# Optimization experiments

Measured on AMD Instinct MI355X. Metric: run time of the kernel, lower is better.

## Reference

```python
import jax, jax.numpy as jnp
import numpy as np

NEG_SLOPE = 0.2  # PyG GATConv default leaky_relu slope
EPS = 1e-16


def setup_inputs() -> dict:
    key = jax.random.key(0)
    ks = jax.random.split(key, 6)
    N, F, H, C, E = 50000, 128, 8, 16, 600000
    node_features = jax.random.normal(ks[0], (N, F), dtype=jnp.float32)
    edge_index = jax.random.randint(ks[1], (2, E), 0, N, dtype=jnp.int64)
    W = jax.random.normal(ks[2], (F, H * C), dtype=jnp.float32) * (1.0 / np.sqrt(F))
    att_src = jax.random.normal(ks[3], (H, C), dtype=jnp.float32)
    att_dst = jax.random.normal(ks[4], (H, C), dtype=jnp.float32)
    bias = jnp.zeros((H * C,), dtype=jnp.float32)
    return {"node_features": node_features, "edge_index": edge_index,
            "W": W, "att_src": att_src, "att_dst": att_dst, "bias": bias}


def reference(node_features, edge_index, W, att_src, att_dst, bias):
    N = node_features.shape[0]
    H, C = att_src.shape
    # Linear transform, split into heads: [N, H, C]
    x = (node_features @ W).reshape(N, H, C)
    # add self loops (PyG default add_self_loops=True)
    loop = jnp.arange(N, dtype=edge_index.dtype)
    src = jnp.concatenate([edge_index[0], loop])  # message source j
    dst = jnp.concatenate([edge_index[1], loop])  # message target i
    # per-node attention logits [N, H]
    a_src = jnp.einsum('nhc,hc->nh', x, att_src)
    a_dst = jnp.einsum('nhc,hc->nh', x, att_dst)
    # edge-wise logits with leaky relu [E, H]
    alpha = jax.nn.leaky_relu(a_src[src] + a_dst[dst], NEG_SLOPE)
    # softmax over incoming edges of each target node (segment softmax)
    amax = jax.ops.segment_max(alpha, dst, num_segments=N)
    alpha = jnp.exp(alpha - amax[dst])
    asum = jax.ops.segment_sum(alpha, dst, num_segments=N)
    alpha = alpha / (asum[dst] + EPS)
    # weighted scatter-aggregate of source features [N, H, C]
    msgs = x[src] * alpha[:, :, None]
    out = jax.ops.segment_sum(msgs, dst, num_segments=N)
    out = out.reshape(N, H * C) + bias
    # SELU activation; dropout is identity in eval mode
    return jax.nn.selu(out)
```

## Files before the change

kernel.cpp:

```cpp
#include <hip/hip_runtime.h>
#include <hip/hip_fp16.h>

#define LEAKY_SLOPE 0.2f

typedef _Float16 h8 __attribute__((ext_vector_type(8)));
typedef float f32x4 __attribute__((ext_vector_type(4)));

__device__ __forceinline__ float leaky_relu_f(float v) { return v > 0.f ? v : LEAKY_SLOPE * v; }
__device__ __forceinline__ float selu_f(float v) {
    const float sc = 1.0507009873554805f, al = 1.6732632423543772f;
    return v > 0.f ? sc * v : sc * al * expm1f(v);
}

__device__ __forceinline__ int detect_is64_wave(const int* __restrict__ e32) {
    int v = e32[2 * (threadIdx.x & 63) + 1];
    unsigned long long b = __ballot(v != 0);
    return b == 0ull ? 1 : 0;
}

__device__ __forceinline__ int edge_at(const void* edges, long long idx, int is64) {
    return is64 ? (int)((const long long*)edges)[idx] : ((const int*)edges)[idx];
}

__global__ void prep_kernel(int* __restrict__ deg, int n,
                            const float* __restrict__ W, _Float16* __restrict__ Wt,
                            int* __restrict__ state, int nstate) {
    int i = blockIdx.x * blockDim.x + threadIdx.x;
    if (i < n) deg[i] = 0;
    if (i < nstate) state[i] = 0;
    if (i < 128 * 128) {
        int k = i >> 7, c = i & 127;
        Wt[c * 128 + k] = (_Float16)W[i];
    }
}

__global__ __launch_bounds__(256) void gemmhist_kernel(
    const float* __restrict__ feats, const _Float16* __restrict__ Wt,
    const float* __restrict__ att_src, const float* __restrict__ att_dst,
    __half* __restrict__ xh, float* __restrict__ a_src, float* __restrict__ a_dst,
    int N, int gemmBlocks,
    const void* __restrict__ edges, long long E,
    int* __restrict__ deg, int* __restrict__ rank) {
    __shared__ __align__(16) _Float16 Af[64][136];
    __shared__ __align__(16) _Float16 Bt[128][136];
    const int t = threadIdx.x;

    if ((int)blockIdx.x >= gemmBlocks) {
        int is64 = detect_is64_wave((const int*)edges);
        long long hstride = (long long)(gridDim.x - gemmBlocks) * blockDim.x;
        for (long long e = (long long)((int)blockIdx.x - gemmBlocks) * blockDim.x + t;
             e < E; e += hstride) {
            int dst = edge_at(edges, E + e, is64);
            rank[e] = atomicAdd(&deg[dst], 1);
        }
        return;
    }

    const int bid = blockIdx.x;
    if (bid == 0) {
        if (t < 64) *(__half2*)&xh[(long long)N * 128 + 2 * t] = __floats2half2_rn(0.f, 0.f);
        if (t < 8) a_src[N * 8 + t] = -1e30f;
    }

    {
        const float4* F4 = (const float4*)feats;
#pragma unroll
        for (int i = 0; i < 8; i++) {
            int q = t + i * 256;
            int row = q >> 5;
            int c = (q & 31) * 4;
            int r_abs = bid * 64 + row;
            if (r_abs >= N) r_abs = N - 1;
            float4 v = F4[(long long)r_abs * 32 + (q & 31)];
            union { _Float16 h[4]; uint2 u; } tmp;
            tmp.h[0] = (_Float16)v.x; tmp.h[1] = (_Float16)v.y;
            tmp.h[2] = (_Float16)v.z; tmp.h[3] = (_Float16)v.w;
            *(uint2*)&Af[row][c] = tmp.u;
        }
    }
    {
        const uint4* Wt4 = (const uint4*)Wt;
#pragma unroll
        for (int i = 0; i < 8; i++) {
            int q = t + i * 256;
            int c = q >> 4;
            int k0 = (q & 15) * 8;
            *(uint4*)&Bt[c][k0] = Wt4[q];
        }
    }
    __syncthreads();

    const int l = t & 63;
    const int w = t >> 6;
    const int lr = l & 15;
    const int lg = l >> 4;

    f32x4 acc[8];
#pragma unroll
    for (int n = 0; n < 8; n++) acc[n] = (f32x4){0.f, 0.f, 0.f, 0.f};

#pragma unroll
    for (int kk = 0; kk < 4; kk++) {
        const int k0 = kk * 32 + lg * 8;
        h8 a = *(const h8*)&Af[16 * w + lr][k0];
#pragma unroll
        for (int n = 0; n < 8; n++) {
            h8 b = *(const h8*)&Bt[16 * n + lr][k0];
            acc[n] = __builtin_amdgcn_mfma_f32_16x16x32_f16(a, b, acc[n], 0, 0, 0);
        }
    }

    const int rbase = bid * 64 + 16 * w + lg * 4;
#pragma unroll
    for (int n = 0; n < 8; n++) {
        float asv = att_src[n * 16 + lr];
        float adv = att_dst[n * 16 + lr];
#pragma unroll
        for (int r = 0; r < 4; r++) {
            int row_abs = rbase + r;
            float v = acc[n][r];
            if (row_abs < N) xh[(long long)row_abs * 128 + 16 * n + lr] = (__half)v;
            float ps = v * asv;
            float pd = v * adv;
            ps += __shfl_xor(ps, 1); ps += __shfl_xor(ps, 2);
            ps += __shfl_xor(ps, 4); ps += __shfl_xor(ps, 8);
            pd += __shfl_xor(pd, 1); pd += __shfl_xor(pd, 2);
            pd += __shfl_xor(pd, 4); pd += __shfl_xor(pd, 8);
            if (lr == n && row_abs < N) {
                a_src[row_abs * 8 + n] = ps;
                a_dst[row_abs * 8 + n] = pd;
            }
        }
    }
}

__global__ __launch_bounds__(256) void scanlb_kernel(const int* __restrict__ deg,
                                                     int* __restrict__ offs,
                                                     int* __restrict__ csr,
                                                     int* __restrict__ state,
                                                     int N, int nb) {
    __shared__ int lds[256];
    __shared__ int s_excl;
    const int b = blockIdx.x, t = threadIdx.x;
    const int base = b * 1024 + t * 4;

    int d[4], v[4], s = 0;
#pragma unroll
    for (int i = 0; i < 4; i++) {
        d[i] = (base + i < N) ? deg[base + i] : 0;
        v[i] = (d[i] + 7) & ~7;
        s += v[i];
    }
    lds[t] = s;
    __syncthreads();
    for (int off = 1; off < 256; off <<= 1) {
        int u = (t >= off) ? lds[t - off] : 0;
        __syncthreads();
        lds[t] += u;
        __syncthreads();
    }
    const int total = lds[255];
    const int local_excl = (t == 0) ? 0 : lds[t - 1];

    if (t == 0) {
        if (b == 0) {
            __hip_atomic_store(&state[0], (total << 2) | 2, __ATOMIC_RELEASE,
                               __HIP_MEMORY_SCOPE_AGENT);
            s_excl = 0;
        } else {
            __hip_atomic_store(&state[b], (total << 2) | 1, __ATOMIC_RELEASE,
                               __HIP_MEMORY_SCOPE_AGENT);
            int excl = 0;
            for (int j = b - 1; j >= 0; j--) {
                int st;
                do {
                    st = __hip_atomic_load(&state[j], __ATOMIC_ACQUIRE,
                                           __HIP_MEMORY_SCOPE_AGENT);
                } while ((st & 3) == 0);
                excl += st >> 2;
                if ((st & 3) == 2) break;
            }
            __hip_atomic_store(&state[b], ((excl + total) << 2) | 2, __ATOMIC_RELEASE,
                               __HIP_MEMORY_SCOPE_AGENT);
            s_excl = excl;
        }
    }
    __syncthreads();
    const int excl = s_excl;

    int run = excl + local_excl;
#pragma unroll
    for (int i = 0; i < 4; i++) {
        int idx = base + i;
        if (idx < N) {
            offs[idx] = run;
            for (int q = run + d[i]; q < run + v[i]; q++) csr[q] = N;
        }
        run += v[i];
    }
    if (b == nb - 1 && t == 255) offs[N] = excl + total;
}

__global__ void scatter_kernel(const void* __restrict__ edges, long long E,
                               const int* __restrict__ offs, const int* __restrict__ rank,
                               int* __restrict__ csr) {
    int is64 = detect_is64_wave((const int*)edges);
    long long stride = (long long)gridDim.x * blockDim.x;
    for (long long e = (long long)blockIdx.x * blockDim.x + threadIdx.x; e < E; e += stride) {
        int src = edge_at(edges, e, is64);
        int dst = edge_at(edges, E + e, is64);
        csr[offs[dst] + rank[e]] = src;
    }
}

__global__ __launch_bounds__(256) void agg_kernel(const __half* __restrict__ xh,
                                                  const float* __restrict__ a_src,
                                                  const float* __restrict__ a_dst,
                                                  const int* __restrict__ offs,
                                                  const int* __restrict__ csr,
                                                  const float* __restrict__ bias,
                                                  float* __restrict__ out, int N) {
    int node = blockIdx.x * 4 + (threadIdx.x >> 6);
    if (node >= N) return;
    int l = threadIdx.x & 63;
    int h8i = l & 7;
    int e8 = l >> 3;
    int hg = l >> 3;

    float ad_w = a_dst[node * 8 + h8i];
    float wself = expf(leaky_relu_f(a_src[node * 8 + h8i] + ad_w));
    float spart = (e8 == 0) ? wself : 0.f;

    float wself_h = __shfl(wself, hg);
    float2 xs = __half22float2(*(const __half2*)&xh[(long long)node * 128 + 2 * l]);
    float accx = wself_h * xs.x;
    float accy = wself_h * xs.y;

    int beg = offs[node], end = offs[node + 1];
    int srcv = 0;
    float w = 0.f;
    if (beg < end) {
        srcv = csr[beg + e8];
        w = expf(leaky_relu_f(a_src[srcv * 8 + h8i] + ad_w));
    }
    for (int p = beg; p < end; p += 8) {
        spart += w;
        int pn = p + 8;
        int srcv_n = 0;
        float asv_n = 0.f;
        bool more = pn < end;
        if (more) {
            srcv_n = csr[pn + e8];
            asv_n = a_src[srcv_n * 8 + h8i];
        }
        float wcur = w;
        int srcv_c = srcv;
#pragma unroll
        for (int e = 0; e < 8; e++) {
            int src = __shfl(srcv_c, e * 8);
            float we = __shfl(wcur, e * 8 + hg);
            float2 xv = __half22float2(*(const __half2*)&xh[(long long)src * 128 + 2 * l]);
            accx = fmaf(we, xv.x, accx);
            accy = fmaf(we, xv.y, accy);
        }
        w = more ? expf(leaky_relu_f(asv_n + ad_w)) : 0.f;
        srcv = srcv_n;
    }
    spart += __shfl_xor(spart, 8);
    spart += __shfl_xor(spart, 16);
    spart += __shfl_xor(spart, 32);
    float s = __shfl(spart, hg);
    float inv = 1.f / (s + 1e-16f);

    float2 b = *(const float2*)&bias[2 * l];
    float2 o;
    o.x = selu_f(fmaf(accx, inv, b.x));
    o.y = selu_f(fmaf(accy, inv, b.y));
    *(float2*)&out[(long long)node * 128 + 2 * l] = o;
}

extern "C" void kernel_launch(void* const* d_in, const int* in_sizes, int n_in,
                              void* d_out, int out_size, void* d_ws, size_t ws_size,
                              hipStream_t stream) {
    const float* feats   = (const float*)d_in[0];
    const void*  edges   = d_in[1];
    const float* W       = (const float*)d_in[2];
    const float* att_src = (const float*)d_in[3];
    const float* att_dst = (const float*)d_in[4];
    const float* bias    = (const float*)d_in[5];

    const int N = in_sizes[0] / 128;
    const long long E = in_sizes[1] / 2;
    const long long fillE = E + 7LL * N;
    float* out = (float*)d_out;

    char* ws = (char*)d_ws;
    __half*   xh    = (__half*)ws;   ws += (size_t)(N + 1) * 128 * 2;
    float*    a_src = (float*)ws;    ws += (size_t)(N + 1) * 8 * 4;
    float*    a_dst = (float*)ws;    ws += (size_t)N * 8 * 4;
    _Float16* Wt    = (_Float16*)ws; ws += 128 * 128 * 2;
    int*      deg   = (int*)ws;      ws += (size_t)N * 4;
    int*      offs  = (int*)ws;      ws += (size_t)(N + 1) * 4;
    int*      rank  = (int*)ws;      ws += (size_t)E * 4;
    int*      state = (int*)ws;      ws += 64 * 4;
    int*      csr   = (int*)ws;      ws += (size_t)fillE * 4;

    const int nb = (N + 1023) / 1024;
    const int gemmBlocks = (N + 63) / 64;
    const int histBlocks = 1024;

    prep_kernel<<<(N + 255) / 256, 256, 0, stream>>>(deg, N, W, Wt, state, nb + 1);
    gemmhist_kernel<<<gemmBlocks + histBlocks, 256, 0, stream>>>(
        feats, Wt, att_src, att_dst, xh, a_src, a_dst, N, gemmBlocks, edges, E, deg, rank);
    scanlb_kernel<<<nb, 256, 0, stream>>>(deg, offs, csr, state, N, nb);
    scatter_kernel<<<2048, 256, 0, stream>>>(edges, E, offs, rank, csr);
    agg_kernel<<<(N + 3) / 4, 256, 0, stream>>>(xh, a_src, a_dst, offs, csr, bias, out, N);
}
```

Baseline: 109.7 us.

## Split fused GEMM/histogram kernel into separate launches, reorder after scan

Replaces the combined kernel, in which some blocks ran the dense GEMM and the rest ran the degree histogram, with two separate kernels. The histogram kernel runs first with 2048 blocks, then the scan, then the GEMM before the scatter. The split removes the mixed-role block scheduling and the large shared-memory footprint that the histogram blocks carried for no use. In exchange it adds a kernel launch and loses the overlap between GEMM and atomic histogram work.

New measurement: 119.0 us. 1.08x slower.

```diff
diff --git a/kernel.cpp b/kernel.cpp
--- a/kernel.cpp
+++ b/kernel.cpp
@@ -34,30 +34,28 @@
     }
 }
 
-__global__ __launch_bounds__(256) void gemmhist_kernel(
-    const float* __restrict__ feats, const _Float16* __restrict__ Wt,
-    const float* __restrict__ att_src, const float* __restrict__ att_dst,
-    __half* __restrict__ xh, float* __restrict__ a_src, float* __restrict__ a_dst,
-    int N, int gemmBlocks,
-    const void* __restrict__ edges, long long E,
-    int* __restrict__ deg, int* __restrict__ rank) {
+__global__ void hist_kernel(const void* __restrict__ edges, long long E,
+                            int* __restrict__ deg, int* __restrict__ rank) {
+    int is64 = detect_is64_wave((const int*)edges);
+    long long stride = (long long)gridDim.x * blockDim.x;
+    for (long long e = (long long)blockIdx.x * blockDim.x + threadIdx.x; e < E; e += stride) {
+        int dst = edge_at(edges, E + e, is64);
+        rank[e] = atomicAdd(&deg[dst], 1);
+    }
+}
+
+__global__ __launch_bounds__(256) void gemm_kernel(const float* __restrict__ feats,
+                                                   const _Float16* __restrict__ Wt,
+                                                   const float* __restrict__ att_src,
+                                                   const float* __restrict__ att_dst,
+                                                   __half* __restrict__ xh,
+                                                   float* __restrict__ a_src,
+                                                   float* __restrict__ a_dst, int N) {
     __shared__ __align__(16) _Float16 Af[64][136];
     __shared__ __align__(16) _Float16 Bt[128][136];
     const int t = threadIdx.x;
 
-    if ((int)blockIdx.x >= gemmBlocks) {
-        int is64 = detect_is64_wave((const int*)edges);
-        long long hstride = (long long)(gridDim.x - gemmBlocks) * blockDim.x;
-        for (long long e = (long long)((int)blockIdx.x - gemmBlocks) * blockDim.x + t;
-             e < E; e += hstride) {
-            int dst = edge_at(edges, E + e, is64);
-            rank[e] = atomicAdd(&deg[dst], 1);
-        }
-        return;
-    }
-
-    const int bid = blockIdx.x;
-    if (bid == 0) {
+    if (blockIdx.x == 0) {
         if (t < 64) *(__half2*)&xh[(long long)N * 128 + 2 * t] = __floats2half2_rn(0.f, 0.f);
         if (t < 8) a_src[N * 8 + t] = -1e30f;
     }
@@ -69,7 +67,7 @@
             int q = t + i * 256;
             int row = q >> 5;
             int c = (q & 31) * 4;
-            int r_abs = bid * 64 + row;
+            int r_abs = blockIdx.x * 64 + row;
             if (r_abs >= N) r_abs = N - 1;
             float4 v = F4[(long long)r_abs * 32 + (q & 31)];
             union { _Float16 h[4]; uint2 u; } tmp;
@@ -110,7 +108,7 @@
         }
     }
 
-    const int rbase = bid * 64 + 16 * w + lg * 4;
+    const int rbase = blockIdx.x * 64 + 16 * w + lg * 4;
 #pragma unroll
     for (int n = 0; n < 8; n++) {
         float asv = att_src[n * 16 + lr];
@@ -306,13 +304,10 @@
     int*      csr   = (int*)ws;      ws += (size_t)fillE * 4;
 
     const int nb = (N + 1023) / 1024;
-    const int gemmBlocks = (N + 63) / 64;
-    const int histBlocks = 1024;
-
     prep_kernel<<<(N + 255) / 256, 256, 0, stream>>>(deg, N, W, Wt, state, nb + 1);
-    gemmhist_kernel<<<gemmBlocks + histBlocks, 256, 0, stream>>>(
-        feats, Wt, att_src, att_dst, xh, a_src, a_dst, N, gemmBlocks, edges, E, deg, rank);
+    hist_kernel<<<2048, 256, 0, stream>>>(edges, E, deg, rank);
     scanlb_kernel<<<nb, 256, 0, stream>>>(deg, offs, csr, state, N, nb);
+    gemm_kernel<<<(N + 63) / 64, 256, 0, stream>>>(feats, Wt, att_src, att_dst, xh, a_src, a_dst, N);
     scatter_kernel<<<2048, 256, 0, stream>>>(edges, E, offs, rank, csr);
     agg_kernel<<<(N + 3) / 4, 256, 0, stream>>>(xh, a_src, a_dst, offs, csr, bias, out, N);
 }
```
